# Kernel optimization log

Hardware: AMD Instinct MI355X
Metric: run time of the kernel (lower is better)

## Reference

```python
import jax, jax.numpy as jnp
import numpy as np

B, N, D, K = 32, 2048, 512, 256
NEG_SLOPE = 0.01  # torch LeakyReLU default


def setup_inputs() -> dict:
    key = jax.random.key(0)
    k1, k2, k3, k4, k5, k6 = jax.random.split(key, 6)
    s = 1.0 / np.sqrt(D)
    sk = 1.0 / np.sqrt(K)
    return {
        "vI": jax.random.normal(k1, (B, N, D), dtype=jnp.float32),
        "vQ": jax.random.normal(k2, (B, D), dtype=jnp.float32),
        "Wi": jax.random.uniform(k3, (D, K), minval=-s, maxval=s, dtype=jnp.float32),
        "Wq": jax.random.uniform(k4, (D, K), minval=-s, maxval=s, dtype=jnp.float32),
        "bq": jax.random.uniform(k5, (K,), minval=-s, maxval=s, dtype=jnp.float32),
        "Wp": jax.random.uniform(k6, (K, 1), minval=-sk, maxval=sk, dtype=jnp.float32),
        "bp": jnp.zeros((1,), dtype=jnp.float32),
    }


def reference(vI, vQ, Wi, Wq, bq, Wp, bp):
    # vI: [B,N,D], vQ: [B,D]
    vIp = jnp.einsum("bnd,dk->bnk", vI, Wi)          # [B,N,K] (no bias)
    vQp = vQ @ Wq + bq                                  # [B,K]
    ha = jax.nn.leaky_relu(vIp + vQp[:, None, :], NEG_SLOPE)  # [B,N,K]
    scores = jnp.einsum("bnk,k->bn", ha, Wp[:, 0]) + bp[0]    # [B,N]
    pi = jax.nn.softmax(scores, axis=-1)                # [B,N]
    vI_attn = jnp.einsum("bn,bnk->bk", pi, vIp)        # [B,K]
    return vI_attn + vQp
```

## Files before the change

kernel.cpp:

```cpp
#include <hip/hip_runtime.h>

#define CB 32
#define CN 2048
#define CD 512
#define CK 256

typedef __bf16 bf16x8 __attribute__((ext_vector_type(8)));
typedef float  f32x4  __attribute__((ext_vector_type(4)));

__device__ __forceinline__ unsigned pk2bf(float a, float b) {
    union { float f; unsigned u; } x, y; x.f = a; y.f = b;
    unsigned ru = x.u + 0x7fffu + ((x.u >> 16) & 1u);
    unsigned rv = y.u + 0x7fffu + ((y.u >> 16) & 1u);
    return (ru >> 16) | (rv & 0xffff0000u);
}

__device__ __forceinline__ unsigned short bf16r(float a) {
    union { float f; unsigned u; } x; x.f = a;
    unsigned r = x.u + 0x7fffu + ((x.u >> 16) & 1u);
    return (unsigned short)(r >> 16);
}

__device__ __forceinline__ void glds16(const void* g, void* l) {
    __builtin_amdgcn_global_load_lds(
        (const __attribute__((address_space(1))) void*)g,
        (__attribute__((address_space(3))) void*)l, 16, 0, 0);
}

__global__ __launch_bounds__(256) void prep_kernel(
        const float* __restrict__ Wi, const float* __restrict__ Wq,
        const float* __restrict__ vQ, const float* __restrict__ bq,
        unsigned short* __restrict__ WiT, float* __restrict__ vQpP)
{
    const int tid = threadIdx.x;
    if (blockIdx.x < 32) {
        const int t = blockIdx.x;
        const int d0 = (t >> 2) * 64, k0 = (t & 3) * 64;
        __shared__ float sT[64][68];
        const int r = tid >> 4, c4 = (tid & 15) * 4;
        #pragma unroll
        for (int i = 0; i < 4; ++i) {
            float4 v = *reinterpret_cast<const float4*>(
                Wi + (size_t)(d0 + r + i * 16) * CK + k0 + c4);
            *reinterpret_cast<float4*>(&sT[r + i * 16][c4]) = v;
        }
        __syncthreads();
        const int k = tid >> 2, dg = (tid & 3) * 16;
        unsigned short __attribute__((aligned(16))) ov[16];
        #pragma unroll
        for (int j = 0; j < 16; ++j) ov[j] = bf16r(sT[dg + j][k]);
        unsigned short* dst = WiT + (size_t)(k0 + k) * CD + d0 + dg;
        *reinterpret_cast<uint4*>(dst)     = *reinterpret_cast<const uint4*>(&ov[0]);
        *reinterpret_cast<uint4*>(dst + 8) = *reinterpret_cast<const uint4*>(&ov[8]);
    } else {
        const int bb = blockIdx.x - 32;
        const int b = bb >> 3, j = bb & 7;
        __shared__ float sq[64];
        if (tid < 64) sq[tid] = vQ[b * CD + j * 64 + tid];
        __syncthreads();
        float acc = (j == 0) ? bq[tid] : 0.f;
        const float* wq = Wq + (size_t)j * 64 * CK + tid;
        #pragma unroll
        for (int d = 0; d < 64; d += 8) {
            float wv[8];
            #pragma unroll
            for (int u = 0; u < 8; ++u) wv[u] = wq[(d + u) * CK];
            #pragma unroll
            for (int u = 0; u < 8; ++u) acc += sq[d + u] * wv[u];
        }
        vQpP[(size_t)bb * CK + tid] = acc;
    }
}

__global__ __launch_bounds__(256, 2) void scores_fused_kernel(
        const float* __restrict__ vI, const unsigned short* __restrict__ WiT,
        const float* __restrict__ vQpP, const float* __restrict__ Wp,
        float* __restrict__ numP, float* __restrict__ Zp, float* __restrict__ mP)
{
    constexpr int BM = 128, BK = 64;
    __shared__ __align__(16) unsigned short sB[2][CK * BK];
    float* sred = (float*)sB[0];
    float* sS   = ((float*)sB[0]) + 512;
    float* sW   = ((float*)sB[0]) + 640;

    const int tid  = threadIdx.x;
    const int b    = blockIdx.y;
    const int n0   = blockIdx.x * BM;
    const int wave = tid >> 6;
    const int lane = tid & 63;
    const int col  = lane & 15;
    const int quad = lane >> 4;

    const float* vIb   = vI + ((size_t)b * CN + n0) * CD;
    const float* aBase = vIb + (size_t)col * CD + quad * 8;

    int gBoff[8];
    #pragma unroll
    for (int t = 0; t < 8; ++t) {
        int row = wave * 64 + t * 8 + (lane >> 3);
        int c   = (lane & 7) ^ (row & 7);
        gBoff[t] = row * CD + c * 8;
    }

    f32x4 acc[8][4];
    #pragma unroll
    for (int mt = 0; mt < 8; ++mt)
        #pragma unroll
        for (int kt = 0; kt < 4; ++kt)
            acc[mt][kt] = (f32x4){0.f, 0.f, 0.f, 0.f};

    #pragma unroll
    for (int i = 0; i < 8; ++i)
        glds16(WiT + gBoff[i], (unsigned short*)sB[0] + (wave * 8 + i) * 512);
    __syncthreads();

    for (int t = 0; t < 8; ++t) {
        const int d0 = t * BK;
        const unsigned short* bufC = sB[t & 1];

        f32x4 a0[8], a1[8];
        #pragma unroll
        for (int mt = 0; mt < 8; ++mt) {
            const float* p = aBase + (size_t)(mt * 16) * CD + d0;
            a0[mt] = *reinterpret_cast<const f32x4*>(p);
            a1[mt] = *reinterpret_cast<const f32x4*>(p + 4);
        }
        if (t < 7) {
            #pragma unroll
            for (int i = 0; i < 8; ++i)
                glds16(WiT + gBoff[i] + d0 + BK,
                       (unsigned short*)sB[(t + 1) & 1] + (wave * 8 + i) * 512);
        }
        #pragma unroll
        for (int s = 0; s < 2; ++s) {
            if (s == 1) {
                #pragma unroll
                for (int mt = 0; mt < 8; ++mt) {
                    const float* p = aBase + (size_t)(mt * 16) * CD + d0 + 32;
                    a0[mt] = *reinterpret_cast<const f32x4*>(p);
                    a1[mt] = *reinterpret_cast<const f32x4*>(p + 4);
                }
            }
            const int slot = (4 * s + quad) ^ (col & 7);
            bf16x8 bfr[4];
            #pragma unroll
            for (int kt = 0; kt < 4; ++kt) {
                int R = wave * 64 + kt * 16 + col;
                bfr[kt] = *reinterpret_cast<const bf16x8*>(bufC + R * 64 + slot * 8);
            }
            #pragma unroll
            for (int mt = 0; mt < 8; ++mt) {
                union { unsigned u[4]; bf16x8 v; } af;
                af.u[0] = pk2bf(a0[mt].x, a0[mt].y);
                af.u[1] = pk2bf(a0[mt].z, a0[mt].w);
                af.u[2] = pk2bf(a1[mt].x, a1[mt].y);
                af.u[3] = pk2bf(a1[mt].z, a1[mt].w);
                #pragma unroll
                for (int kt = 0; kt < 4; ++kt)
                    acc[mt][kt] = __builtin_amdgcn_mfma_f32_16x16x32_bf16(
                        af.v, bfr[kt], acc[mt][kt], 0, 0, 0);
            }
        }
        __syncthreads();
    }

    float vq[4], wp[4];
    #pragma unroll
    for (int kt = 0; kt < 4; ++kt) {
        int k = wave * 64 + kt * 16 + col;
        float a = 0.f;
        #pragma unroll
        for (int j = 0; j < 8; ++j) a += vQpP[(b * 8 + j) * CK + k];
        vq[kt] = a;
        wp[kt] = Wp[k];
    }
    float sp[8][4];
    #pragma unroll
    for (int mt = 0; mt < 8; ++mt)
        #pragma unroll
        for (int r = 0; r < 4; ++r) {
            float s = 0.f;
            #pragma unroll
            for (int kt = 0; kt < 4; ++kt) {
                float v = acc[mt][kt][r] + vq[kt];
                v = v > 0.f ? v : 0.01f * v;
                s += v * wp[kt];
            }
            sp[mt][r] = s;
        }
    #pragma unroll
    for (int off = 1; off < 16; off <<= 1)
        #pragma unroll
        for (int mt = 0; mt < 8; ++mt)
            #pragma unroll
            for (int r = 0; r < 4; ++r)
                sp[mt][r] += __shfl_xor(sp[mt][r], off);

    __syncthreads();
    if (col == 0) {
        #pragma unroll
        for (int mt = 0; mt < 8; ++mt)
            #pragma unroll
            for (int r = 0; r < 4; ++r)
                sred[wave * 128 + mt * 16 + quad * 4 + r] = sp[mt][r];
    }
    __syncthreads();
    if (tid < BM)
        sS[tid] = sred[tid] + sred[128 + tid] + sred[256 + tid] + sred[384 + tid];
    __syncthreads();

    float m = -1e30f;
    #pragma unroll 8
    for (int i = 0; i < BM; ++i) m = fmaxf(m, sS[i]);
    if (tid < BM) sW[tid] = __expf(sS[tid] - m);
    __syncthreads();
    float z = (tid < BM) ? sW[tid] : 0.f;
    #pragma unroll
    for (int off = 32; off > 0; off >>= 1) z += __shfl_xor(z, off);
    if (lane == 0) sS[wave] = z;
    __syncthreads();
    const int pidx = b * 16 + blockIdx.x;
    if (tid == 0) {
        Zp[pidx] = sS[0] + sS[1] + sS[2] + sS[3];
        mP[pidx] = m;
    }

    float nk[4] = {0.f, 0.f, 0.f, 0.f};
    #pragma unroll
    for (int mt = 0; mt < 8; ++mt)
        #pragma unroll
        for (int r = 0; r < 4; ++r) {
            float w = sW[mt * 16 + quad * 4 + r];
            #pragma unroll
            for (int kt = 0; kt < 4; ++kt)
                nk[kt] += w * acc[mt][kt][r];
        }
    #pragma unroll
    for (int kt = 0; kt < 4; ++kt) {
        nk[kt] += __shfl_xor(nk[kt], 16);
        nk[kt] += __shfl_xor(nk[kt], 32);
    }
    if (quad == 0) {
        #pragma unroll
        for (int kt = 0; kt < 4; ++kt)
            numP[(size_t)pidx * CK + wave * 64 + kt * 16 + col] = nk[kt];
    }
}

__global__ __launch_bounds__(256) void finalize_kernel(
        const float* __restrict__ numP, const float* __restrict__ Zp,
        const float* __restrict__ mP, const float* __restrict__ vQpP,
        float* __restrict__ out)
{
    const int b = blockIdx.x, tid = threadIdx.x;
    float M = -1e30f;
    #pragma unroll
    for (int j = 0; j < 16; ++j) M = fmaxf(M, mP[b * 16 + j]);
    float w[16]; float Zt = 0.f;
    #pragma unroll
    for (int j = 0; j < 16; ++j) {
        w[j] = __expf(mP[b * 16 + j] - M);
        Zt += w[j] * Zp[b * 16 + j];
    }
    const float inv = 1.f / Zt;
    float s = 0.f;
    #pragma unroll
    for (int j = 0; j < 16; ++j) s += w[j] * numP[(size_t)(b * 16 + j) * CK + tid];
    float vq = 0.f;
    #pragma unroll
    for (int j = 0; j < 8; ++j) vq += vQpP[(size_t)(b * 8 + j) * CK + tid];
    out[b * CK + tid] = s * inv + vq;
}

extern "C" void kernel_launch(void* const* d_in, const int* in_sizes, int n_in,
                              void* d_out, int out_size, void* d_ws, size_t ws_size,
                              hipStream_t stream)
{
    const float* vI = (const float*)d_in[0];
    const float* vQ = (const float*)d_in[1];
    const float* Wi = (const float*)d_in[2];
    const float* Wq = (const float*)d_in[3];
    const float* bq = (const float*)d_in[4];
    const float* Wp = (const float*)d_in[5];
    float* out = (float*)d_out;

    char* ws = (char*)d_ws;
    float*          vQpP = (float*)(ws);
    unsigned short* WiT  = (unsigned short*)(ws + 262144);
    float*          numP = (float*)(ws + 524288);
    float*          Zp   = (float*)(ws + 524288 + 524288);
    float*          mP   = (float*)(ws + 1048576 + 2048);

    prep_kernel        <<<288, 256, 0, stream>>>(Wi, Wq, vQ, bq, WiT, vQpP);
    scores_fused_kernel<<<dim3(CN / 128, CB), 256, 0, stream>>>(vI, WiT, vQpP, Wp,
                                                                numP, Zp, mP);
    finalize_kernel    <<<CB, 256, 0, stream>>>(numP, Zp, mP, vQpP, out);
}
```

Before: 248.3 us.

## Split GEMM tile across waves by rows instead of K columns

Each wave now owns 32 rows of the 128-row tile and all 256 output columns (2x16 MFMA tiles) rather than 64 columns over all 128 rows. This cuts redundant fp32 global loads and bf16 conversions of vI across the four waves. The K loop is unrolled by two with prefetch of the next A fragments into registers, and the epilogue now reduces partial numerators across waves through shared memory. The trade-off is more LDS reads of B per wave, which may raise LDS bandwidth pressure, and extra epilogue synchronisation.

```diff
diff --git a/kernel.cpp b/kernel.cpp
--- a/kernel.cpp
+++ b/kernel.cpp
@@ -79,9 +79,12 @@
 {
     constexpr int BM = 128, BK = 64;
     __shared__ __align__(16) unsigned short sB[2][CK * BK];
-    float* sred = (float*)sB[0];
-    float* sS   = ((float*)sB[0]) + 512;
-    float* sW   = ((float*)sB[0]) + 640;
+    float* fb   = (float*)sB[0];
+    float* svq  = fb;
+    float* swp  = fb + 256;
+    float* sS   = fb + 512;
+    float* sW   = fb + 640;
+    float* snum = fb + 768;
 
     const int tid  = threadIdx.x;
     const int b    = blockIdx.y;
@@ -92,96 +95,115 @@
     const int quad = lane >> 4;
 
     const float* vIb   = vI + ((size_t)b * CN + n0) * CD;
-    const float* aBase = vIb + (size_t)col * CD + quad * 8;
+    const float* aBase = vIb + (size_t)(wave * 32 + col) * CD + quad * 8;
 
     int gBoff[8];
     #pragma unroll
-    for (int t = 0; t < 8; ++t) {
-        int row = wave * 64 + t * 8 + (lane >> 3);
+    for (int i = 0; i < 8; ++i) {
+        int row = wave * 64 + i * 8 + (lane >> 3);
         int c   = (lane & 7) ^ (row & 7);
-        gBoff[t] = row * CD + c * 8;
-    }
-
-    f32x4 acc[8][4];
-    #pragma unroll
-    for (int mt = 0; mt < 8; ++mt)
-        #pragma unroll
-        for (int kt = 0; kt < 4; ++kt)
+        gBoff[i] = row * CD + c * 8;
+    }
+
+    f32x4 acc[2][16];
+    #pragma unroll
+    for (int mt = 0; mt < 2; ++mt)
+        #pragma unroll
+        for (int kt = 0; kt < 16; ++kt)
             acc[mt][kt] = (f32x4){0.f, 0.f, 0.f, 0.f};
 
-    #pragma unroll
-    for (int i = 0; i < 8; ++i)
-        glds16(WiT + gBoff[i], (unsigned short*)sB[0] + (wave * 8 + i) * 512);
-    __syncthreads();
-
-    for (int t = 0; t < 8; ++t) {
-        const int d0 = t * BK;
-        const unsigned short* bufC = sB[t & 1];
-
-        f32x4 a0[8], a1[8];
-        #pragma unroll
-        for (int mt = 0; mt < 8; ++mt) {
-            const float* p = aBase + (size_t)(mt * 16) * CD + d0;
-            a0[mt] = *reinterpret_cast<const f32x4*>(p);
-            a1[mt] = *reinterpret_cast<const f32x4*>(p + 4);
-        }
-        if (t < 7) {
-            #pragma unroll
-            for (int i = 0; i < 8; ++i)
-                glds16(WiT + gBoff[i] + d0 + BK,
-                       (unsigned short*)sB[(t + 1) & 1] + (wave * 8 + i) * 512);
-        }
+    f32x4 aA[8], aB2[8];
+
+    auto loadA = [&](f32x4* dst, int d0) {
+        #pragma unroll
+        for (int mt = 0; mt < 2; ++mt)
+            #pragma unroll
+            for (int s = 0; s < 2; ++s) {
+                const float* p = aBase + (size_t)(mt * 16) * CD + d0 + s * 32;
+                dst[mt * 4 + s * 2]     = *reinterpret_cast<const f32x4*>(p);
+                dst[mt * 4 + s * 2 + 1] = *reinterpret_cast<const f32x4*>(p + 4);
+            }
+    };
+    auto stageB = [&](int d0, int buf) {
+        #pragma unroll
+        for (int i = 0; i < 8; ++i)
+            glds16(WiT + gBoff[i] + d0,
+                   (unsigned short*)sB[buf] + (wave * 8 + i) * 512);
+    };
+    auto compute = [&](const f32x4* ar, const unsigned short* bufC) {
+        bf16x8 af[2][2];
+        #pragma unroll
+        for (int mt = 0; mt < 2; ++mt)
+            #pragma unroll
+            for (int s = 0; s < 2; ++s) {
+                union { unsigned u[4]; bf16x8 v; } t;
+                const f32x4 lo = ar[mt * 4 + s * 2], hi = ar[mt * 4 + s * 2 + 1];
+                t.u[0] = pk2bf(lo.x, lo.y); t.u[1] = pk2bf(lo.z, lo.w);
+                t.u[2] = pk2bf(hi.x, hi.y); t.u[3] = pk2bf(hi.z, hi.w);
+                af[mt][s] = t.v;
+            }
         #pragma unroll
         for (int s = 0; s < 2; ++s) {
-            if (s == 1) {
+            const int slot = (4 * s + quad) ^ (col & 7);
+            #pragma unroll
+            for (int kc = 0; kc < 4; ++kc) {
+                bf16x8 bfr[4];
                 #pragma unroll
-                for (int mt = 0; mt < 8; ++mt) {
-                    const float* p = aBase + (size_t)(mt * 16) * CD + d0 + 32;
-                    a0[mt] = *reinterpret_cast<const f32x4*>(p);
-                    a1[mt] = *reinterpret_cast<const f32x4*>(p + 4);
+                for (int u = 0; u < 4; ++u) {
+                    int R = (kc * 4 + u) * 16 + col;
+                    bfr[u] = *reinterpret_cast<const bf16x8*>(bufC + R * 64 + slot * 8);
                 }
+                #pragma unroll
+                for (int u = 0; u < 4; ++u)
+                    #pragma unroll
+                    for (int mt = 0; mt < 2; ++mt)
+                        acc[mt][kc * 4 + u] = __builtin_amdgcn_mfma_f32_16x16x32_bf16(
+                            af[mt][s], bfr[u], acc[mt][kc * 4 + u], 0, 0, 0);
             }
-            const int slot = (4 * s + quad) ^ (col & 7);
-            bf16x8 bfr[4];
-            #pragma unroll
-            for (int kt = 0; kt < 4; ++kt) {
-                int R = wave * 64 + kt * 16 + col;
-                bfr[kt] = *reinterpret_cast<const bf16x8*>(bufC + R * 64 + slot * 8);
-            }
-            #pragma unroll
-            for (int mt = 0; mt < 8; ++mt) {
-                union { unsigned u[4]; bf16x8 v; } af;
-                af.u[0] = pk2bf(a0[mt].x, a0[mt].y);
-                af.u[1] = pk2bf(a0[mt].z, a0[mt].w);
-                af.u[2] = pk2bf(a1[mt].x, a1[mt].y);
-                af.u[3] = pk2bf(a1[mt].z, a1[mt].w);
-                #pragma unroll
-                for (int kt = 0; kt < 4; ++kt)
-                    acc[mt][kt] = __builtin_amdgcn_mfma_f32_16x16x32_bf16(
-                        af.v, bfr[kt], acc[mt][kt], 0, 0, 0);
-            }
-        }
+        }
+    };
+
+    loadA(aA, 0);
+    stageB(0, 0);
+    __syncthreads();
+
+    for (int tt = 0; tt < 4; ++tt) {
+        const int d0 = tt * 128;
+        loadA(aB2, d0 + 64);
+        stageB(d0 + 64, 1);
+        compute(aA, sB[0]);
         __syncthreads();
-    }
-
-    float vq[4], wp[4];
-    #pragma unroll
-    for (int kt = 0; kt < 4; ++kt) {
-        int k = wave * 64 + kt * 16 + col;
+        if (tt < 3) {
+            loadA(aA, d0 + 128);
+            stageB(d0 + 128, 0);
+        }
+        compute(aB2, sB[1]);
+        __syncthreads();
+    }
+
+    {
         float a = 0.f;
         #pragma unroll
-        for (int j = 0; j < 8; ++j) a += vQpP[(b * 8 + j) * CK + k];
-        vq[kt] = a;
-        wp[kt] = Wp[k];
-    }
-    float sp[8][4];
-    #pragma unroll
-    for (int mt = 0; mt < 8; ++mt)
+        for (int j = 0; j < 8; ++j) a += vQpP[(b * 8 + j) * CK + tid];
+        svq[tid] = a;
+        swp[tid] = Wp[tid];
+    }
+    __syncthreads();
+
+    float vq[16], wp[16];
+    #pragma unroll
+    for (int kt = 0; kt < 16; ++kt) {
+        vq[kt] = svq[kt * 16 + col];
+        wp[kt] = swp[kt * 16 + col];
+    }
+    float sp[2][4];
+    #pragma unroll
+    for (int mt = 0; mt < 2; ++mt)
         #pragma unroll
         for (int r = 0; r < 4; ++r) {
             float s = 0.f;
             #pragma unroll
-            for (int kt = 0; kt < 4; ++kt) {
+            for (int kt = 0; kt < 16; ++kt) {
                 float v = acc[mt][kt][r] + vq[kt];
                 v = v > 0.f ? v : 0.01f * v;
                 s += v * wp[kt];
@@ -191,22 +213,17 @@
     #pragma unroll
     for (int off = 1; off < 16; off <<= 1)
         #pragma unroll
-        for (int mt = 0; mt < 8; ++mt)
+        for (int mt = 0; mt < 2; ++mt)
             #pragma unroll
             for (int r = 0; r < 4; ++r)
                 sp[mt][r] += __shfl_xor(sp[mt][r], off);
-
-    __syncthreads();
     if (col == 0) {
         #pragma unroll
-        for (int mt = 0; mt < 8; ++mt)
+        for (int mt = 0; mt < 2; ++mt)
             #pragma unroll
             for (int r = 0; r < 4; ++r)
-                sred[wave * 128 + mt * 16 + quad * 4 + r] = sp[mt][r];
-    }
-    __syncthreads();
-    if (tid < BM)
-        sS[tid] = sred[tid] + sred[128 + tid] + sred[256 + tid] + sred[384 + tid];
+                sS[wave * 32 + mt * 16 + quad * 4 + r] = sp[mt][r];
+    }
     __syncthreads();
 
     float m = -1e30f;
@@ -225,26 +242,33 @@
         mP[pidx] = m;
     }
 
-    float nk[4] = {0.f, 0.f, 0.f, 0.f};
-    #pragma unroll
-    for (int mt = 0; mt < 8; ++mt)
-        #pragma unroll
-        for (int r = 0; r < 4; ++r) {
-            float w = sW[mt * 16 + quad * 4 + r];
-            #pragma unroll
-            for (int kt = 0; kt < 4; ++kt)
-                nk[kt] += w * acc[mt][kt][r];
-        }
-    #pragma unroll
-    for (int kt = 0; kt < 4; ++kt) {
-        nk[kt] += __shfl_xor(nk[kt], 16);
-        nk[kt] += __shfl_xor(nk[kt], 32);
+    float w8[2][4];
+    #pragma unroll
+    for (int mt = 0; mt < 2; ++mt)
+        #pragma unroll
+        for (int r = 0; r < 4; ++r)
+            w8[mt][r] = sW[wave * 32 + mt * 16 + quad * 4 + r];
+    float nk[16];
+    #pragma unroll
+    for (int kt = 0; kt < 16; ++kt) {
+        float s = 0.f;
+        #pragma unroll
+        for (int mt = 0; mt < 2; ++mt)
+            #pragma unroll
+            for (int r = 0; r < 4; ++r)
+                s += w8[mt][r] * acc[mt][kt][r];
+        s += __shfl_xor(s, 16);
+        s += __shfl_xor(s, 32);
+        nk[kt] = s;
     }
     if (quad == 0) {
         #pragma unroll
-        for (int kt = 0; kt < 4; ++kt)
-            numP[(size_t)pidx * CK + wave * 64 + kt * 16 + col] = nk[kt];
-    }
+        for (int kt = 0; kt < 16; ++kt)
+            snum[wave * 256 + kt * 16 + col] = nk[kt];
+    }
+    __syncthreads();
+    numP[(size_t)pidx * CK + tid] =
+        snum[tid] + snum[256 + tid] + snum[512 + tid] + snum[768 + tid];
 }
 
 __global__ __launch_bounds__(256) void finalize_kernel(
```

After: 223.6 us. 1.11x faster.
